# Performance work log

Measured on AMD Instinct MI355X. Metric: run time of the kernel, lower is better.

## Reference

```python
import jax, jax.numpy as jnp
import numpy as np

ALPHA = 300.0  # attractor strength (exp variant: exp(-alpha*|dx|^gamma)*dx, gamma=2)


def setup_inputs() -> dict:
    key = jax.random.key(0)
    k0, k1, k2, k3 = jax.random.split(key, 4)
    n, c, h, w = 4, 256, 128, 128
    mlp_dim, n_attractors, n_bins = 128, 16, 64
    x = jax.random.normal(k0, (n, c, h, w), jnp.float32)
    b_prev = jax.random.uniform(k1, (n, n_bins, h, w), jnp.float32)  # bin centers
    w1 = jax.random.normal(k2, (mlp_dim, c), jnp.float32) * 0.02
    b1 = jnp.zeros((mlp_dim,), jnp.float32)
    w2 = jax.random.normal(k3, (n_attractors, mlp_dim), jnp.float32) * 0.02
    b2 = jnp.zeros((n_attractors,), jnp.float32)
    return {"x": x, "b_prev": b_prev, "w1": w1, "b1": b1, "w2": w2, "b2": b2}


def reference(x, b_prev, w1, b1, w2, b2):
    # 1x1 conv MLP head: Conv2d(c->mlp) -> ReLU -> Conv2d(mlp->n_attractors) -> Softplus
    hfeat = jax.nn.relu(jnp.einsum('nchw,oc->nohw', x, w1) + b1[None, :, None, None])
    A = jax.nn.softplus(jnp.einsum('nchw,oc->nohw', hfeat, w2) + b2[None, :, None, None])
    # b_prev interpolated to (h, w) == identity here (same spatial size)
    b_centers = b_prev
    # dx: [n, n_attractors, n_bins, h, w]
    dx = A[:, :, None, :, :] - b_centers[:, None, :, :, :]
    # exp attractor with gamma=2: exp(-alpha*dx^2) * dx, summed over attractors ('sum' kind)
    delta_c = jnp.sum(jnp.exp(-ALPHA * dx * dx) * dx, axis=1)
    b_new_centers = b_centers + delta_c
    return (b_new_centers, b_new_centers)
```

## Files before the change

### kernel.cpp

```cpp
#include <hip/hip_runtime.h>
#include <hip/hip_bf16.h>
#include <stdint.h>


#define HW 16384
#define ALPHA 300.0f

typedef short bf16x8_t __attribute__((ext_vector_type(8)));
typedef float f32x4_t __attribute__((ext_vector_type(4)));
typedef unsigned int u32x4_t __attribute__((ext_vector_type(4)));

__device__ __forceinline__ unsigned short f2bf(float f) {
  unsigned int u = __builtin_bit_cast(unsigned int, f);
  u += 0x7fffu + ((u >> 16) & 1u);
  return (unsigned short)(u >> 16);
}
__device__ __forceinline__ unsigned int pack2(float a, float b) {
  return (unsigned int)f2bf(a) | ((unsigned int)f2bf(b) << 16);
}

__global__ void zoed_prep(const float* __restrict__ w1,
                          const float* __restrict__ w2,
                          unsigned short* __restrict__ blob) {
  int i = blockIdx.x * 256 + threadIdx.x;
  if (i < 32768) {
    int o = i >> 8, c = i & 255;
    float v = w1[i];
    int idx = (c >> 5) * 4096 + o * 32 + ((((c >> 3) & 3) ^ (o & 3)) << 3) + (c & 7);
    blob[idx] = f2bf(v);
  } else {
    int i2 = i - 32768;
    int a = i2 >> 7, o = i2 & 127;
    float v = w2[i2];
    int idx = 32768 + (o >> 5) * 512 + a * 32 + ((((o >> 3) & 3) ^ (a & 3)) << 3) + (o & 7);
    blob[idx] = f2bf(v);
  }
}

__global__ __launch_bounds__(256, 4) void zoed_fused(
    const float* __restrict__ x, const float* __restrict__ bprev,
    const float* __restrict__ b1, const float* __restrict__ b2,
    const unsigned short* __restrict__ wblob, float* __restrict__ out) {
  __shared__ __align__(16) char smem[20480];
  char* hid = smem;
  char* Albuf = smem + 16384;

  const int t = threadIdx.x;
  const int lane = t & 63;
  const int l15 = lane & 15;
  const int quad = lane >> 4;
  const int wv = t >> 6;
  const int wm = wv & 1;
  const int wn = wv >> 1;
  const int sw = ((quad ^ (lane & 3)) << 4);

  const int blk = blockIdx.x;
  const int n = blk >> 8;
  const int p0 = (blk & 255) << 6;

  const int sp = t & 63;
  const int sg = t >> 6;

  const float* xsbase = x + (size_t)(n * 256 + sg * 8) * HW + p0 + sp;
  float xr[4][8];
#pragma unroll
  for (int c = 0; c < 4; c++)
#pragma unroll
    for (int j = 0; j < 8; j++)
      xr[c][j] = xsbase[(size_t)(c * 32 + j) * HW];

  const char* wbase = (const char*)wblob + (wm * 64 + l15) * 64 + sw;
  bf16x8_t afn[4];
#pragma unroll
  for (int tm = 0; tm < 4; tm++)
    afn[tm] = *(const bf16x8_t*)(wbase + tm * 1024);

  f32x4_t acc[4][2];
#pragma unroll
  for (int i = 0; i < 4; i++)
#pragma unroll
    for (int j = 0; j < 2; j++) acc[i][j] = (f32x4_t){0.f, 0.f, 0.f, 0.f};

#pragma unroll
  for (int kb = 0; kb < 8; ++kb) {
    char* xb = smem + (kb & 1) * 4096;
    bf16x8_t afc[4];
#pragma unroll
    for (int tm = 0; tm < 4; tm++) afc[tm] = afn[tm];
    if (kb < 7) {
#pragma unroll
      for (int tm = 0; tm < 4; tm++)
        afn[tm] = *(const bf16x8_t*)(wbase + (kb + 1) * 8192 + tm * 1024);
    }
    {
      u32x4_t v = {pack2(xr[kb & 3][0], xr[kb & 3][1]),
                   pack2(xr[kb & 3][2], xr[kb & 3][3]),
                   pack2(xr[kb & 3][4], xr[kb & 3][5]),
                   pack2(xr[kb & 3][6], xr[kb & 3][7])};
      *(u32x4_t*)(xb + sp * 64 + ((sg ^ (sp & 3)) << 4)) = v;
    }
    if (kb < 4) {
#pragma unroll
      for (int j = 0; j < 8; j++)
        xr[kb & 3][j] = xsbase[(size_t)((kb + 4) * 32 + j) * HW];
    }
    __syncthreads();
    bf16x8_t bfm[2];
#pragma unroll
    for (int tn = 0; tn < 2; tn++)
      bfm[tn] = *(const bf16x8_t*)(xb + (wn * 32 + tn * 16 + l15) * 64 + sw);
#pragma unroll
    for (int tm = 0; tm < 4; tm++)
#pragma unroll
      for (int tn = 0; tn < 2; tn++)
        acc[tm][tn] = __builtin_amdgcn_mfma_f32_16x16x32_bf16(
            afc[tm], bfm[tn], acc[tm][tn], 0, 0, 0);
  }

  const int ap = t & 63;
  const int grp = t >> 6;
  size_t obase = (size_t)n * 64 * HW + (size_t)(grp * 16) * HW + (size_t)(p0 + ap);
  const float* bp = bprev + obase;
  float bpr[16];
#pragma unroll
  for (int b = 0; b < 16; b++) bpr[b] = bp[(size_t)b * HW];
  bf16x8_t a2[4];
#pragma unroll
  for (int kc = 0; kc < 4; kc++)
    a2[kc] = *(const bf16x8_t*)((const char*)wblob + 65536 + kc * 1024 +
                                l15 * 64 + sw);

  __syncthreads();
#pragma unroll
  for (int tm = 0; tm < 4; tm++) {
    f32x4_t b1v = *(const f32x4_t*)(b1 + wm * 64 + tm * 16 + quad * 4);
    int kc = wm * 2 + (tm >> 1);
    int g = (tm & 1) * 2 + (quad >> 1);
    int off8 = (quad & 1) * 8;
#pragma unroll
    for (int tn = 0; tn < 2; tn++) {
      f32x4_t h = acc[tm][tn] + b1v;
      h[0] = fmaxf(h[0], 0.f);
      h[1] = fmaxf(h[1], 0.f);
      h[2] = fmaxf(h[2], 0.f);
      h[3] = fmaxf(h[3], 0.f);
      int prow = wn * 32 + tn * 16 + l15;
      unsigned int* dst = (unsigned int*)(hid + kc * 4096 + prow * 64 +
                                          ((g ^ (prow & 3)) << 4) + off8);
      dst[0] = pack2(h[0], h[1]);
      dst[1] = pack2(h[2], h[3]);
    }
  }
  __syncthreads();
  {
    f32x4_t acc2 = (f32x4_t){0.f, 0.f, 0.f, 0.f};
    const int prow = wv * 16 + l15;
#pragma unroll
    for (int kc = 0; kc < 4; kc++) {
      bf16x8_t bh = *(const bf16x8_t*)(hid + kc * 4096 + prow * 64 + sw);
      acc2 = __builtin_amdgcn_mfma_f32_16x16x32_bf16(a2[kc], bh, acc2, 0, 0, 0);
    }
    f32x4_t b2v = *(const f32x4_t*)(b2 + quad * 4);
    f32x4_t z = acc2 + b2v;
    f32x4_t spv;
#pragma unroll
    for (int r = 0; r < 4; r++) {
      float zz = z[r];
      spv[r] = fmaxf(zz, 0.f) + log1pf(__expf(-fabsf(zz)));
    }
    *(f32x4_t*)(Albuf + prow * 64 + ((quad ^ (prow & 3)) << 4)) = spv;
  }
  __syncthreads();
  {
    float Av[16];
#pragma unroll
    for (int q = 0; q < 4; q++) {
      f32x4_t v = *(const f32x4_t*)(Albuf + ap * 64 + ((q ^ (ap & 3)) << 4));
      Av[q * 4 + 0] = v[0];
      Av[q * 4 + 1] = v[1];
      Av[q * 4 + 2] = v[2];
      Av[q * 4 + 3] = v[3];
    }
    float* o1 = out + obase;
    float* o2 = out + (size_t)4 * 64 * HW + obase;
#pragma unroll
    for (int b = 0; b < 16; b++) {
      float c = bpr[b];
      float d0 = 0.f, d1 = 0.f;
#pragma unroll
      for (int a = 0; a < 8; a++) {
        float dx = Av[a] - c;
        float e = __expf(dx * dx * -ALPHA);
        d0 = fmaf(e, dx, d0);
      }
#pragma unroll
      for (int a = 8; a < 16; a++) {
        float dx = Av[a] - c;
        float e = __expf(dx * dx * -ALPHA);
        d1 = fmaf(e, dx, d1);
      }
      float r = c + (d0 + d1);
      __builtin_nontemporal_store(r, o1 + (size_t)b * HW);
      __builtin_nontemporal_store(r, o2 + (size_t)b * HW);
    }
  }
}

extern "C" void kernel_launch(void* const* d_in, const int* in_sizes, int n_in,
                              void* d_out, int out_size, void* d_ws,
                              size_t ws_size, hipStream_t stream) {
  const float* x = (const float*)d_in[0];
  const float* bprev = (const float*)d_in[1];
  const float* w1 = (const float*)d_in[2];
  const float* b1 = (const float*)d_in[3];
  const float* w2 = (const float*)d_in[4];
  const float* b2 = (const float*)d_in[5];
  float* outp = (float*)d_out;
  unsigned short* blob = (unsigned short*)d_ws;

  zoed_prep<<<136, 256, 0, stream>>>(w1, w2, blob);
  zoed_fused<<<1024, 256, 0, stream>>>(x, bprev, b1, b2, blob, outp);
}
```

Before: 133.9 us.

## Split fused kernel into MLP and attractor kernels with per-wave MLP tiles

Splits the single fused kernel into two: an MLP kernel where each wave independently computes 16 pixels (B fragments built straight from registers, no shared-memory staging of x or block barriers), and an attractor kernel that reads A from a workspace buffer alongside b_prev. This removes the cross-wave syncs and LDS round trip for x, and drops the swizzle from the weight layout. In exchange it adds an extra launch and a global write plus read of the A tensor (4x16x16384 floats). Weights are now loaded per-MFMA from global/L2 instead of being prefetched.

```diff
diff --git a/kernel.cpp b/kernel.cpp
--- a/kernel.cpp
+++ b/kernel.cpp
@@ -8,7 +8,6 @@
 
 typedef short bf16x8_t __attribute__((ext_vector_type(8)));
 typedef float f32x4_t __attribute__((ext_vector_type(4)));
-typedef unsigned int u32x4_t __attribute__((ext_vector_type(4)));
 
 __device__ __forceinline__ unsigned short f2bf(float f) {
   unsigned int u = __builtin_bit_cast(unsigned int, f);
@@ -25,184 +24,134 @@
   int i = blockIdx.x * 256 + threadIdx.x;
   if (i < 32768) {
     int o = i >> 8, c = i & 255;
-    float v = w1[i];
-    int idx = (c >> 5) * 4096 + o * 32 + ((((c >> 3) & 3) ^ (o & 3)) << 3) + (c & 7);
-    blob[idx] = f2bf(v);
+    blob[(c >> 5) * 4096 + o * 32 + (c & 31)] = f2bf(w1[i]);
   } else {
     int i2 = i - 32768;
     int a = i2 >> 7, o = i2 & 127;
-    float v = w2[i2];
-    int idx = 32768 + (o >> 5) * 512 + a * 32 + ((((o >> 3) & 3) ^ (a & 3)) << 3) + (o & 7);
-    blob[idx] = f2bf(v);
+    blob[32768 + (o >> 5) * 512 + a * 32 + (o & 31)] = f2bf(w2[i2]);
   }
 }
 
-__global__ __launch_bounds__(256, 4) void zoed_fused(
-    const float* __restrict__ x, const float* __restrict__ bprev,
-    const float* __restrict__ b1, const float* __restrict__ b2,
-    const unsigned short* __restrict__ wblob, float* __restrict__ out) {
-  __shared__ __align__(16) char smem[20480];
-  char* hid = smem;
-  char* Albuf = smem + 16384;
-
+__global__ __launch_bounds__(256, 4) void zoed_mlp(
+    const float* __restrict__ x, const float* __restrict__ b1,
+    const float* __restrict__ b2, const unsigned short* __restrict__ wblob,
+    float* __restrict__ A) {
+  __shared__ __align__(16) char smem[16384];
   const int t = threadIdx.x;
   const int lane = t & 63;
   const int l15 = lane & 15;
   const int quad = lane >> 4;
   const int wv = t >> 6;
-  const int wm = wv & 1;
-  const int wn = wv >> 1;
-  const int sw = ((quad ^ (lane & 3)) << 4);
+  char* hb = smem + wv * 4096;
 
-  const int blk = blockIdx.x;
-  const int n = blk >> 8;
-  const int p0 = (blk & 255) << 6;
+  const int wid = blockIdx.x * 4 + wv;
+  const int px0 = wid * 16;
+  const int n = px0 >> 14;
+  const int p = px0 & 16383;
 
-  const int sp = t & 63;
-  const int sg = t >> 6;
+  const float* xb = x + (size_t)(n * 256 + quad * 8) * HW + p + l15;
+  float xr[8][8];
+#pragma unroll
+  for (int kc = 0; kc < 8; kc++)
+#pragma unroll
+    for (int j = 0; j < 8; j++) xr[kc][j] = xb[(size_t)(kc * 32 + j) * HW];
 
-  const float* xsbase = x + (size_t)(n * 256 + sg * 8) * HW + p0 + sp;
-  float xr[4][8];
+  f32x4_t acc[8];
 #pragma unroll
-  for (int c = 0; c < 4; c++)
+  for (int m = 0; m < 8; m++) acc[m] = (f32x4_t){0.f, 0.f, 0.f, 0.f};
+
+  const char* wb1 = (const char*)wblob + l15 * 64 + quad * 16;
 #pragma unroll
-    for (int j = 0; j < 8; j++)
-      xr[c][j] = xsbase[(size_t)(c * 32 + j) * HW];
-
-  const char* wbase = (const char*)wblob + (wm * 64 + l15) * 64 + sw;
-  bf16x8_t afn[4];
+  for (int kc = 0; kc < 8; kc++) {
+    bf16x8_t bfrag;
+    unsigned int* bu = (unsigned int*)&bfrag;
+    bu[0] = pack2(xr[kc][0], xr[kc][1]);
+    bu[1] = pack2(xr[kc][2], xr[kc][3]);
+    bu[2] = pack2(xr[kc][4], xr[kc][5]);
+    bu[3] = pack2(xr[kc][6], xr[kc][7]);
 #pragma unroll
-  for (int tm = 0; tm < 4; tm++)
-    afn[tm] = *(const bf16x8_t*)(wbase + tm * 1024);
-
-  f32x4_t acc[4][2];
-#pragma unroll
-  for (int i = 0; i < 4; i++)
-#pragma unroll
-    for (int j = 0; j < 2; j++) acc[i][j] = (f32x4_t){0.f, 0.f, 0.f, 0.f};
+    for (int m = 0; m < 8; m++) {
+      bf16x8_t af = *(const bf16x8_t*)(wb1 + kc * 8192 + m * 1024);
+      acc[m] = __builtin_amdgcn_mfma_f32_16x16x32_bf16(af, bfrag, acc[m], 0, 0, 0);
+    }
+  }
 
 #pragma unroll
-  for (int kb = 0; kb < 8; ++kb) {
-    char* xb = smem + (kb & 1) * 4096;
-    bf16x8_t afc[4];
-#pragma unroll
-    for (int tm = 0; tm < 4; tm++) afc[tm] = afn[tm];
-    if (kb < 7) {
-#pragma unroll
-      for (int tm = 0; tm < 4; tm++)
-        afn[tm] = *(const bf16x8_t*)(wbase + (kb + 1) * 8192 + tm * 1024);
-    }
-    {
-      u32x4_t v = {pack2(xr[kb & 3][0], xr[kb & 3][1]),
-                   pack2(xr[kb & 3][2], xr[kb & 3][3]),
-                   pack2(xr[kb & 3][4], xr[kb & 3][5]),
-                   pack2(xr[kb & 3][6], xr[kb & 3][7])};
-      *(u32x4_t*)(xb + sp * 64 + ((sg ^ (sp & 3)) << 4)) = v;
-    }
-    if (kb < 4) {
-#pragma unroll
-      for (int j = 0; j < 8; j++)
-        xr[kb & 3][j] = xsbase[(size_t)((kb + 4) * 32 + j) * HW];
-    }
-    __syncthreads();
-    bf16x8_t bfm[2];
-#pragma unroll
-    for (int tn = 0; tn < 2; tn++)
-      bfm[tn] = *(const bf16x8_t*)(xb + (wn * 32 + tn * 16 + l15) * 64 + sw);
-#pragma unroll
-    for (int tm = 0; tm < 4; tm++)
-#pragma unroll
-      for (int tn = 0; tn < 2; tn++)
-        acc[tm][tn] = __builtin_amdgcn_mfma_f32_16x16x32_bf16(
-            afc[tm], bfm[tn], acc[tm][tn], 0, 0, 0);
+  for (int m = 0; m < 8; m++) {
+    f32x4_t b1v = *(const f32x4_t*)(b1 + m * 16 + quad * 4);
+    f32x4_t h = acc[m] + b1v;
+    h[0] = fmaxf(h[0], 0.f);
+    h[1] = fmaxf(h[1], 0.f);
+    h[2] = fmaxf(h[2], 0.f);
+    h[3] = fmaxf(h[3], 0.f);
+    int G = m * 2 + (quad >> 1);
+    unsigned int* dst = (unsigned int*)(hb + l15 * 256 + ((G ^ (l15 & 3)) << 4) +
+                                        (quad & 1) * 8);
+    dst[0] = pack2(h[0], h[1]);
+    dst[1] = pack2(h[2], h[3]);
   }
 
-  const int ap = t & 63;
-  const int grp = t >> 6;
-  size_t obase = (size_t)n * 64 * HW + (size_t)(grp * 16) * HW + (size_t)(p0 + ap);
+  f32x4_t acc2 = (f32x4_t){0.f, 0.f, 0.f, 0.f};
+  const char* wb2 = (const char*)wblob + 65536 + l15 * 64 + quad * 16;
+#pragma unroll
+  for (int kc2 = 0; kc2 < 4; kc2++) {
+    bf16x8_t a2 = *(const bf16x8_t*)(wb2 + kc2 * 1024);
+    int G = kc2 * 4 + quad;
+    bf16x8_t bh = *(const bf16x8_t*)(hb + l15 * 256 + ((G ^ (l15 & 3)) << 4));
+    acc2 = __builtin_amdgcn_mfma_f32_16x16x32_bf16(a2, bh, acc2, 0, 0, 0);
+  }
+  f32x4_t b2v = *(const f32x4_t*)(b2 + quad * 4);
+  float* Ab = A + (size_t)(n * 16 + quad * 4) * HW + p + l15;
+#pragma unroll
+  for (int r = 0; r < 4; r++) {
+    float zz = acc2[r] + b2v[r];
+    float sp = fmaxf(zz, 0.f) + log1pf(__expf(-fabsf(zz)));
+    Ab[(size_t)r * HW] = sp;
+  }
+}
+
+__global__ __launch_bounds__(256, 4) void zoed_attr(
+    const float* __restrict__ bprev, const float* __restrict__ A,
+    float* __restrict__ out) {
+  const int t = threadIdx.x;
+  const int blk = blockIdx.x;
+  const int P = (blk & 255) * 256 + t;
+  const int bg = blk >> 8;
+  const int n = P >> 14;
+  const int p = P & 16383;
+
+  const float* Ab = A + (size_t)(n * 16) * HW + p;
+  float Av[16];
+#pragma unroll
+  for (int a = 0; a < 16; a++) Av[a] = Ab[(size_t)a * HW];
+
+  size_t obase = (size_t)(n * 64 + bg * 16) * HW + p;
   const float* bp = bprev + obase;
   float bpr[16];
 #pragma unroll
   for (int b = 0; b < 16; b++) bpr[b] = bp[(size_t)b * HW];
-  bf16x8_t a2[4];
+
+  float* o1 = out + obase;
+  float* o2 = out + (size_t)(4 * 64) * HW + obase;
 #pragma unroll
-  for (int kc = 0; kc < 4; kc++)
-    a2[kc] = *(const bf16x8_t*)((const char*)wblob + 65536 + kc * 1024 +
-                                l15 * 64 + sw);
-
-  __syncthreads();
+  for (int b = 0; b < 16; b++) {
+    float c = bpr[b];
+    float d0 = 0.f, d1 = 0.f;
 #pragma unroll
-  for (int tm = 0; tm < 4; tm++) {
-    f32x4_t b1v = *(const f32x4_t*)(b1 + wm * 64 + tm * 16 + quad * 4);
-    int kc = wm * 2 + (tm >> 1);
-    int g = (tm & 1) * 2 + (quad >> 1);
-    int off8 = (quad & 1) * 8;
+    for (int a = 0; a < 8; a++) {
+      float dx = Av[a] - c;
+      float e = __expf(dx * dx * -ALPHA);
+      d0 = fmaf(e, dx, d0);
+    }
 #pragma unroll
-    for (int tn = 0; tn < 2; tn++) {
-      f32x4_t h = acc[tm][tn] + b1v;
-      h[0] = fmaxf(h[0], 0.f);
-      h[1] = fmaxf(h[1], 0.f);
-      h[2] = fmaxf(h[2], 0.f);
-      h[3] = fmaxf(h[3], 0.f);
-      int prow = wn * 32 + tn * 16 + l15;
-      unsigned int* dst = (unsigned int*)(hid + kc * 4096 + prow * 64 +
-                                          ((g ^ (prow & 3)) << 4) + off8);
-      dst[0] = pack2(h[0], h[1]);
-      dst[1] = pack2(h[2], h[3]);
+    for (int a = 8; a < 16; a++) {
+      float dx = Av[a] - c;
+      float e = __expf(dx * dx * -ALPHA);
+      d1 = fmaf(e, dx, d1);
     }
-  }
-  __syncthreads();
-  {
-    f32x4_t acc2 = (f32x4_t){0.f, 0.f, 0.f, 0.f};
-    const int prow = wv * 16 + l15;
-#pragma unroll
-    for (int kc = 0; kc < 4; kc++) {
-      bf16x8_t bh = *(const bf16x8_t*)(hid + kc * 4096 + prow * 64 + sw);
-      acc2 = __builtin_amdgcn_mfma_f32_16x16x32_bf16(a2[kc], bh, acc2, 0, 0, 0);
-    }
-    f32x4_t b2v = *(const f32x4_t*)(b2 + quad * 4);
-    f32x4_t z = acc2 + b2v;
-    f32x4_t spv;
-#pragma unroll
-    for (int r = 0; r < 4; r++) {
-      float zz = z[r];
-      spv[r] = fmaxf(zz, 0.f) + log1pf(__expf(-fabsf(zz)));
-    }
-    *(f32x4_t*)(Albuf + prow * 64 + ((quad ^ (prow & 3)) << 4)) = spv;
-  }
-  __syncthreads();
-  {
-    float Av[16];
-#pragma unroll
-    for (int q = 0; q < 4; q++) {
-      f32x4_t v = *(const f32x4_t*)(Albuf + ap * 64 + ((q ^ (ap & 3)) << 4));
-      Av[q * 4 + 0] = v[0];
-      Av[q * 4 + 1] = v[1];
-      Av[q * 4 + 2] = v[2];
-      Av[q * 4 + 3] = v[3];
-    }
-    float* o1 = out + obase;
-    float* o2 = out + (size_t)4 * 64 * HW + obase;
-#pragma unroll
-    for (int b = 0; b < 16; b++) {
-      float c = bpr[b];
-      float d0 = 0.f, d1 = 0.f;
-#pragma unroll
-      for (int a = 0; a < 8; a++) {
-        float dx = Av[a] - c;
-        float e = __expf(dx * dx * -ALPHA);
-        d0 = fmaf(e, dx, d0);
-      }
-#pragma unroll
-      for (int a = 8; a < 16; a++) {
-        float dx = Av[a] - c;
-        float e = __expf(dx * dx * -ALPHA);
-        d1 = fmaf(e, dx, d1);
-      }
-      float r = c + (d0 + d1);
-      __builtin_nontemporal_store(r, o1 + (size_t)b * HW);
-      __builtin_nontemporal_store(r, o2 + (size_t)b * HW);
-    }
+    float r = c + (d0 + d1);
+    __builtin_nontemporal_store(r, o1 + (size_t)b * HW);
+    __builtin_nontemporal_store(r, o2 + (size_t)b * HW);
   }
 }
 
@@ -216,8 +165,11 @@
   const float* w2 = (const float*)d_in[4];
   const float* b2 = (const float*)d_in[5];
   float* outp = (float*)d_out;
+
   unsigned short* blob = (unsigned short*)d_ws;
+  float* Abuf = (float*)((char*)d_ws + (1 << 20));
 
   zoed_prep<<<136, 256, 0, stream>>>(w1, w2, blob);
-  zoed_fused<<<1024, 256, 0, stream>>>(x, bprev, b1, b2, blob, outp);
+  zoed_mlp<<<1024, 256, 0, stream>>>(x, b1, b2, blob, Abuf);
+  zoed_attr<<<1024, 256, 0, stream>>>(bprev, Abuf, outp);
 }
```

Result: slower. 156.7 us (+17.1%).
